# Optimization experiments

Hardware: AMD Instinct MI355X
Metric: run time of the kernel (lower is better)

The kernel has to match this reference:

```python
import jax, jax.numpy as jnp
import numpy as np

N_NODES = 100000


def gcn_conv(x, src, dst, W, b, n_nodes):
    """PyG GCNConv: add self-loops, symmetric deg^{-1/2} norm, gather-scatter."""
    h = x @ W  # [N, out]
    # add self-loops (fixed shapes)
    loop = jnp.arange(n_nodes, dtype=src.dtype)
    s = jnp.concatenate([src, loop])
    d = jnp.concatenate([dst, loop])
    # degree on destination (includes self-loop)
    deg = jax.ops.segment_sum(jnp.ones_like(d, dtype=h.dtype), d, num_segments=n_nodes)
    dinv = jnp.where(deg > 0, jax.lax.rsqrt(deg), 0.0)
    norm = dinv[s] * dinv[d]  # [E+N]
    msg = h[s] * norm[:, None]  # gather + scale, [E+N, out]
    out = jax.ops.segment_sum(msg, d, num_segments=n_nodes)  # scatter-add
    return out + b


def setup_inputs() -> dict:
    key = jax.random.key(0)
    ks = jax.random.split(key, 10)
    n, in_d, hid, out_d, e = N_NODES, 64, 128, 64, 1600000
    x = jax.random.normal(ks[0], (n, in_d), dtype=jnp.float32)
    edge_index = jax.random.randint(ks[1], (2, e), 0, n, dtype=jnp.int64)
    s = 0.05
    return {
        "x": x,
        "edge_index": edge_index,
        "W1": jax.random.normal(ks[2], (in_d, hid), dtype=jnp.float32) * s,
        "b1": jnp.zeros((hid,), dtype=jnp.float32),
        "W2": jax.random.normal(ks[3], (hid, out_d), dtype=jnp.float32) * s,
        "b2": jnp.zeros((out_d,), dtype=jnp.float32),
        "Wd": jax.random.normal(ks[4], (out_d, 1), dtype=jnp.float32) * s,
        "bd": jnp.zeros((1,), dtype=jnp.float32),
        "Wp": jax.random.normal(ks[5], (out_d, 1), dtype=jnp.float32) * s,
        "bp": jnp.zeros((1,), dtype=jnp.float32),
    }


def reference(x, edge_index, W1, b1, W2, b2, Wd, bd, Wp, bp):
    src, dst = edge_index[0], edge_index[1]
    n = x.shape[0]
    h = jax.nn.relu(gcn_conv(x, src, dst, W1, b1, n))
    h = jax.nn.relu(gcn_conv(h, src, dst, W2, b2, n))
    duration_out = h @ Wd + bd  # [N, 1]
    phase_out = h @ Wp + bp     # [N, 1]
    return (duration_out, phase_out)
```

## Files before the change

kernel.cpp:

```cpp
#include <hip/hip_runtime.h>
#include <cstdint>
#include <cstddef>


#define MAXC 512
#define CAP  6144
#define SEG  3456
#define GPAD 16

typedef __attribute__((ext_vector_type(8))) short bf16x8;
typedef __attribute__((ext_vector_type(4))) float f32x4;

__device__ __forceinline__ float blo(unsigned int u) {
  return __uint_as_float(u << 16);
}
__device__ __forceinline__ float bhi(unsigned int u) {
  return __uint_as_float(u & 0xffff0000u);
}
__device__ __forceinline__ unsigned short f2b(float f) {
  unsigned int u = __float_as_uint(f);
  unsigned int r = u + 0x7fffu + ((u >> 16) & 1u);
  return (unsigned short)(r >> 16);
}

__global__ __launch_bounds__(256) void k_cast(const float* __restrict__ x,
                                              const float* __restrict__ dinv,
                                              unsigned int* __restrict__ xh,
                                              int n16) {
  int i = blockIdx.x * 256 + threadIdx.x;
  if (i >= n16) return;
  float di = dinv[i >> 4];
  float4 v = reinterpret_cast<const float4*>(x)[i];
  uint2 o;
  o.x = (unsigned int)f2b(v.x * di) | ((unsigned int)f2b(v.y * di) << 16);
  o.y = (unsigned int)f2b(v.z * di) | ((unsigned int)f2b(v.w * di) << 16);
  reinterpret_cast<uint2*>(xh)[i] = o;
}

__global__ void k_binit(int* __restrict__ gcur, int nc) {
  int b = blockIdx.x * 256 + threadIdx.x;
  if (b < nc) gcur[b * GPAD] = b * CAP;
}

__global__ __launch_bounds__(256) void k_pass1(const int* __restrict__ src,
                                               const int* __restrict__ dst,
                                               int* __restrict__ gcur,
                                               int* __restrict__ P,
                                               int E, int nc, int seg) {
  __shared__ int hist[MAXC];
  __shared__ int lofs[MAXC];
  __shared__ int base[MAXC];
  __shared__ int sbuf[SEG];
  __shared__ unsigned short dbuf[SEG];
  __shared__ int ssc[256];
  int tid = threadIdx.x;
  int start = blockIdx.x * seg;
  int end = min(E, start + seg);
  int cnt = end - start;
  if (cnt <= 0) return;
  for (int i = tid; i < MAXC; i += 256) hist[i] = 0;
  __syncthreads();
  for (int i = start + tid; i < end; i += 256)
    atomicAdd(&hist[dst[i] >> 8], 1);
  __syncthreads();
  int p0 = hist[2 * tid], p1 = hist[2 * tid + 1];
  int ps = p0 + p1;
  ssc[tid] = ps;
  __syncthreads();
  for (int off = 1; off < 256; off <<= 1) {
    int t = (tid >= off) ? ssc[tid - off] : 0;
    __syncthreads();
    ssc[tid] += t;
    __syncthreads();
  }
  int pe = ssc[tid] - ps;
  lofs[2 * tid] = pe;
  lofs[2 * tid + 1] = pe + p0;
  __syncthreads();
  for (int b = tid; b < nc; b += 256) {
    int h = hist[b];
    base[b] = (h ? atomicAdd(&gcur[b * GPAD], h) : 0) - lofs[b];
  }
  __syncthreads();
  for (int i = tid; i < MAXC; i += 256) hist[i] = lofs[i];
  __syncthreads();
  for (int i = start + tid; i < end; i += 256) {
    int d = dst[i];
    int b = d >> 8;
    int r = atomicAdd(&hist[b], 1);
    sbuf[r] = src[i] | ((d & 255) << 17);
    dbuf[r] = (unsigned short)b;
  }
  __syncthreads();
  for (int j = tid; j < cnt; j += 256) {
    P[base[dbuf[j]] + j] = sbuf[j];
  }
}

__global__ __launch_bounds__(256) void k_pass2(const int* __restrict__ P,
                                               const int* __restrict__ gcur,
                                               int* __restrict__ rs,
                                               int* __restrict__ c,
                                               float* __restrict__ dinv,
                                               int* __restrict__ col, int N) {
  __shared__ int sh[256];
  __shared__ int lcur[256];
  int tid = threadIdx.x;
  int node0 = blockIdx.x << 8;
  int begin = blockIdx.x * CAP;
  int end = gcur[blockIdx.x * GPAD];
  sh[tid] = 0;
  __syncthreads();
  for (int i = begin + tid; i < end; i += 256)
    atomicAdd(&sh[P[i] >> 17], 1);
  __syncthreads();
  int s = sh[tid];
  for (int off = 1; off < 256; off <<= 1) {
    int t = (tid >= off) ? sh[tid - off] : 0;
    __syncthreads();
    sh[tid] += t;
    __syncthreads();
  }
  int excl = sh[tid] - s;
  int node = node0 + tid;
  if (node < N) {
    rs[node] = begin + excl;
    c[node] = s;
    dinv[node] = rsqrtf((float)(s + 1));
  }
  lcur[tid] = begin + excl;
  __syncthreads();
  for (int i = begin + tid; i < end; i += 256) {
    int p = P[i];
    int pos = atomicAdd(&lcur[p >> 17], 1);
    col[pos] = p & 0x1FFFF;
  }
}

__global__ __launch_bounds__(256) void k_pull1(const unsigned int* __restrict__ xh,
                                               const float* __restrict__ x,
                                               const int* __restrict__ rs,
                                               const int* __restrict__ cnt,
                                               const int* __restrict__ col,
                                               const float* __restrict__ dinv,
                                               unsigned int* __restrict__ aggh,
                                               int n) {
  int node = (blockIdx.x * 256 + threadIdx.x) >> 6;
  int lane = threadIdx.x & 63;
  if (node >= n) return;
  int q = lane & 15;
  int grp = lane >> 4;
  int start = rs[node], m = cnt[node];
  const uint2* xr = reinterpret_cast<const uint2*>(xh);
  float4 acc = {0.f, 0.f, 0.f, 0.f};
  for (int base0 = 0; base0 < m; base0 += 64) {
    int lim = min(64, m - base0);
    int idx = (lane < lim) ? col[start + base0 + lane] : 0;
    int nt = lim >> 2;
    int t = 0;
    for (; t + 4 <= nt; t += 4) {
      int e0 = t * 4 + grp, e1 = e0 + 4, e2 = e0 + 8, e3 = e0 + 12;
      int s0 = __shfl(idx, e0), s1 = __shfl(idx, e1);
      int s2 = __shfl(idx, e2), s3 = __shfl(idx, e3);
      uint2 v0 = xr[(size_t)s0 * 16 + q];
      uint2 v1 = xr[(size_t)s1 * 16 + q];
      uint2 v2 = xr[(size_t)s2 * 16 + q];
      uint2 v3 = xr[(size_t)s3 * 16 + q];
      acc.x += (blo(v0.x) + blo(v1.x)) + (blo(v2.x) + blo(v3.x));
      acc.y += (bhi(v0.x) + bhi(v1.x)) + (bhi(v2.x) + bhi(v3.x));
      acc.z += (blo(v0.y) + blo(v1.y)) + (blo(v2.y) + blo(v3.y));
      acc.w += (bhi(v0.y) + bhi(v1.y)) + (bhi(v2.y) + bhi(v3.y));
    }
    for (; t + 2 <= nt; t += 2) {
      int e0 = t * 4 + grp, e1 = e0 + 4;
      int s0 = __shfl(idx, e0), s1 = __shfl(idx, e1);
      uint2 v0 = xr[(size_t)s0 * 16 + q];
      uint2 v1 = xr[(size_t)s1 * 16 + q];
      acc.x += blo(v0.x) + blo(v1.x); acc.y += bhi(v0.x) + bhi(v1.x);
      acc.z += blo(v0.y) + blo(v1.y); acc.w += bhi(v0.y) + bhi(v1.y);
    }
    if (t < nt) {
      int e0 = t * 4 + grp;
      int s0 = __shfl(idx, e0);
      uint2 v0 = xr[(size_t)s0 * 16 + q];
      acc.x += blo(v0.x); acc.y += bhi(v0.x);
      acc.z += blo(v0.y); acc.w += bhi(v0.y);
    }
    for (int j = nt * 4; j < lim; ++j) {
      int s0 = __shfl(idx, j);
      if (grp == (j & 3)) {
        uint2 v0 = xr[(size_t)s0 * 16 + q];
        acc.x += blo(v0.x); acc.y += bhi(v0.x);
        acc.z += blo(v0.y); acc.w += bhi(v0.y);
      }
    }
  }
  acc.x += __shfl_xor(acc.x, 16); acc.y += __shfl_xor(acc.y, 16);
  acc.z += __shfl_xor(acc.z, 16); acc.w += __shfl_xor(acc.w, 16);
  acc.x += __shfl_xor(acc.x, 32); acc.y += __shfl_xor(acc.y, 32);
  acc.z += __shfl_xor(acc.z, 32); acc.w += __shfl_xor(acc.w, 32);
  float di = dinv[node];
  float4 xs = *reinterpret_cast<const float4*>(x + (size_t)node * 64 + q * 4);
  acc.x = fmaf(di, xs.x, acc.x); acc.y = fmaf(di, xs.y, acc.y);
  acc.z = fmaf(di, xs.z, acc.z); acc.w = fmaf(di, xs.w, acc.w);
  if (lane < 16) {
    uint2 o;
    o.x = (unsigned int)f2b(acc.x * di) | ((unsigned int)f2b(acc.y * di) << 16);
    o.y = (unsigned int)f2b(acc.z * di) | ((unsigned int)f2b(acc.w * di) << 16);
    reinterpret_cast<uint2*>(aggh)[(size_t)node * 16 + q] = o;
  }
}

#define OFF_W1T 16384
#define OFF_W2T 32768
#define OFF_H1  49152
__global__ __launch_bounds__(256) void k_gemm12(
    const unsigned int* __restrict__ aggh,
    const float* __restrict__ W1, const float* __restrict__ b1,
    const float* __restrict__ W2, const float* __restrict__ dinv,
    unsigned int* __restrict__ g2h, int n) {
  __shared__ __align__(16) char smem[81920];
  int tid = threadIdx.x;
  int lane = tid & 63;
  int wid = tid >> 6;
  int lr = lane & 15, lg = lane >> 4;
  int wr = wid >> 1, wc = wid & 1;
  {
    int nrow = tid >> 1, h = tid & 1;
    unsigned int pk[16];
#pragma unroll
    for (int q = 0; q < 16; ++q) {
      unsigned short a = f2b(W1[(size_t)(h * 32 + 2 * q) * 128 + nrow]);
      unsigned short bq = f2b(W1[(size_t)(h * 32 + 2 * q + 1) * 128 + nrow]);
      pk[q] = (unsigned int)a | ((unsigned int)bq << 16);
    }
#pragma unroll
    for (int cc = 0; cc < 4; ++cc) {
      uint4 v = make_uint4(pk[cc * 4], pk[cc * 4 + 1], pk[cc * 4 + 2], pk[cc * 4 + 3]);
      int byte = nrow * 128 + ((h * 64 + cc * 16) ^ ((nrow & 7) << 4));
      *reinterpret_cast<uint4*>(smem + OFF_W1T + byte) = v;
    }
  }
  {
    int nrow = tid >> 2, qt = tid & 3;
    unsigned int pk[16];
#pragma unroll
    for (int q = 0; q < 16; ++q) {
      unsigned short a = f2b(W2[(size_t)(qt * 32 + 2 * q) * 64 + nrow]);
      unsigned short bq = f2b(W2[(size_t)(qt * 32 + 2 * q + 1) * 64 + nrow]);
      pk[q] = (unsigned int)a | ((unsigned int)bq << 16);
    }
#pragma unroll
    for (int cc = 0; cc < 4; ++cc) {
      uint4 v = make_uint4(pk[cc * 4], pk[cc * 4 + 1], pk[cc * 4 + 2], pk[cc * 4 + 3]);
      int byte = nrow * 256 + ((qt * 64 + cc * 16) ^ ((nrow & 7) << 4));
      *reinterpret_cast<uint4*>(smem + OFF_W2T + byte) = v;
    }
  }
  float bias[4];
#pragma unroll
  for (int ni = 0; ni < 4; ++ni) bias[ni] = b1[wc * 64 + ni * 16 + lr];

  int ntiles = (n + 127) >> 7;
  for (int tile = blockIdx.x; tile < ntiles; tile += gridDim.x) {
    int row0 = tile << 7;
    __syncthreads();
#pragma unroll
    for (int j = 0; j < 4; ++j) {
      int idx = tid + 256 * j;
      int r = idx >> 3, u = idx & 7;
      uint4 v = make_uint4(0u, 0u, 0u, 0u);
      int row = row0 + r;
      if (row < n) v = reinterpret_cast<const uint4*>(aggh)[(size_t)row * 8 + u];
      int byte = r * 128 + ((u * 16) ^ ((r & 7) << 4));
      *reinterpret_cast<uint4*>(smem + byte) = v;
    }
    __syncthreads();
    f32x4 acc1[4][4];
#pragma unroll
    for (int mi = 0; mi < 4; ++mi)
#pragma unroll
      for (int ni = 0; ni < 4; ++ni) {
        f32x4 z = {0.f, 0.f, 0.f, 0.f};
        acc1[mi][ni] = z;
      }
#pragma unroll
    for (int kk = 0; kk < 2; ++kk) {
      int kb = kk * 64 + lg * 16;
      bf16x8 af[4], bfq[4];
#pragma unroll
      for (int mi = 0; mi < 4; ++mi) {
        int r = wr * 64 + mi * 16 + lr;
        af[mi] = *reinterpret_cast<const bf16x8*>(smem + r * 128 + (kb ^ ((r & 7) << 4)));
      }
#pragma unroll
      for (int ni = 0; ni < 4; ++ni) {
        int nr = wc * 64 + ni * 16 + lr;
        bfq[ni] = *reinterpret_cast<const bf16x8*>(smem + OFF_W1T + nr * 128 + (kb ^ ((nr & 7) << 4)));
      }
#pragma unroll
      for (int mi = 0; mi < 4; ++mi)
#pragma unroll
        for (int ni = 0; ni < 4; ++ni)
          acc1[mi][ni] = __builtin_amdgcn_mfma_f32_16x16x32_bf16(
              af[mi], bfq[ni], acc1[mi][ni], 0, 0, 0);
    }
#pragma unroll
    for (int mi = 0; mi < 4; ++mi) {
      int m0 = wr * 64 + mi * 16 + lg * 4;
#pragma unroll
      for (int ni = 0; ni < 4; ++ni) {
        int kcol = wc * 64 + ni * 16 + lr;
#pragma unroll
        for (int rj = 0; rj < 4; ++rj) {
          float v = fmaxf(acc1[mi][ni][rj] + bias[ni], 0.f);
          int mm = m0 + rj;
          int byte = mm * 256 + ((kcol * 2) ^ ((mm & 15) << 4));
          *reinterpret_cast<unsigned short*>(smem + OFF_H1 + byte) = f2b(v);
        }
      }
    }
    __syncthreads();
    f32x4 acc2[4][2];
#pragma unroll
    for (int mi = 0; mi < 4; ++mi)
#pragma unroll
      for (int ni = 0; ni < 2; ++ni) {
        f32x4 z = {0.f, 0.f, 0.f, 0.f};
        acc2[mi][ni] = z;
      }
#pragma unroll
    for (int kk = 0; kk < 4; ++kk) {
      int kb = kk * 64 + lg * 16;
      bf16x8 af[4], bfq[2];
#pragma unroll
      for (int mi = 0; mi < 4; ++mi) {
        int m = wr * 64 + mi * 16 + lr;
        af[mi] = *reinterpret_cast<const bf16x8*>(smem + OFF_H1 + m * 256 + (kb ^ ((m & 15) << 4)));
      }
#pragma unroll
      for (int ni = 0; ni < 2; ++ni) {
        int nr = wc * 32 + ni * 16 + lr;
        bfq[ni] = *reinterpret_cast<const bf16x8*>(smem + OFF_W2T + nr * 256 + (kb ^ ((nr & 7) << 4)));
      }
#pragma unroll
      for (int mi = 0; mi < 4; ++mi)
#pragma unroll
        for (int ni = 0; ni < 2; ++ni)
          acc2[mi][ni] = __builtin_amdgcn_mfma_f32_16x16x32_bf16(
              af[mi], bfq[ni], acc2[mi][ni], 0, 0, 0);
    }
    __syncthreads();
#pragma unroll
    for (int mi = 0; mi < 4; ++mi) {
      int m0 = wr * 64 + mi * 16 + lg * 4;
#pragma unroll
      for (int ni = 0; ni < 2; ++ni) {
        int nn = wc * 32 + ni * 16 + lr;
#pragma unroll
        for (int rj = 0; rj < 4; ++rj) {
          int mm = m0 + rj;
          int byte = mm * 256 + ((nn * 4) ^ ((mm & 15) << 4));
          *reinterpret_cast<float*>(smem + OFF_H1 + byte) = acc2[mi][ni][rj];
        }
      }
    }
    __syncthreads();
#pragma unroll
    for (int j = 0; j < 8; ++j) {
      int idx = tid + 256 * j;
      int r = idx >> 4, c4 = idx & 15;
      int row = row0 + r;
      if (row < n) {
        float4 v = *reinterpret_cast<const float4*>(
            smem + OFF_H1 + r * 256 + ((c4 * 16) ^ ((r & 15) << 4)));
        float di = dinv[row];
        uint2 o;
        o.x = (unsigned int)f2b(v.x * di) | ((unsigned int)f2b(v.y * di) << 16);
        o.y = (unsigned int)f2b(v.z * di) | ((unsigned int)f2b(v.w * di) << 16);
        reinterpret_cast<uint2*>(g2h)[(size_t)row * 16 + c4] = o;
      }
    }
  }
}

__global__ __launch_bounds__(256) void k_pull2(const unsigned int* __restrict__ g2h,
                                               const int* __restrict__ rs,
                                               const int* __restrict__ cnt,
                                               const int* __restrict__ col,
                                               const float* __restrict__ dinv,
                                               const float* __restrict__ b,
                                               const float* __restrict__ Wd,
                                               const float* __restrict__ Wp,
                                               const float* __restrict__ bd,
                                               const float* __restrict__ bp,
                                               float* __restrict__ out, int n) {
  int node = (blockIdx.x * 256 + threadIdx.x) >> 6;
  int lane = threadIdx.x & 63;
  if (node >= n) return;
  int q = lane & 15;
  int grp = lane >> 4;
  int start = rs[node], m = cnt[node];
  const uint2* gr = reinterpret_cast<const uint2*>(g2h);
  float4 acc = {0.f, 0.f, 0.f, 0.f};
  for (int base0 = 0; base0 < m; base0 += 64) {
    int lim = min(64, m - base0);
    int idx = (lane < lim) ? col[start + base0 + lane] : 0;
    int nt = lim >> 2;
    int t = 0;
    for (; t + 4 <= nt; t += 4) {
      int e0 = t * 4 + grp, e1 = e0 + 4, e2 = e0 + 8, e3 = e0 + 12;
      int s0 = __shfl(idx, e0), s1 = __shfl(idx, e1);
      int s2 = __shfl(idx, e2), s3 = __shfl(idx, e3);
      uint2 v0 = gr[(size_t)s0 * 16 + q];
      uint2 v1 = gr[(size_t)s1 * 16 + q];
      uint2 v2 = gr[(size_t)s2 * 16 + q];
      uint2 v3 = gr[(size_t)s3 * 16 + q];
      acc.x += (blo(v0.x) + blo(v1.x)) + (blo(v2.x) + blo(v3.x));
      acc.y += (bhi(v0.x) + bhi(v1.x)) + (bhi(v2.x) + bhi(v3.x));
      acc.z += (blo(v0.y) + blo(v1.y)) + (blo(v2.y) + blo(v3.y));
      acc.w += (bhi(v0.y) + bhi(v1.y)) + (bhi(v2.y) + bhi(v3.y));
    }
    for (; t + 2 <= nt; t += 2) {
      int e0 = t * 4 + grp, e1 = e0 + 4;
      int s0 = __shfl(idx, e0), s1 = __shfl(idx, e1);
      uint2 v0 = gr[(size_t)s0 * 16 + q];
      uint2 v1 = gr[(size_t)s1 * 16 + q];
      acc.x += blo(v0.x) + blo(v1.x); acc.y += bhi(v0.x) + bhi(v1.x);
      acc.z += blo(v0.y) + blo(v1.y); acc.w += bhi(v0.y) + bhi(v1.y);
    }
    if (t < nt) {
      int e0 = t * 4 + grp;
      int s0 = __shfl(idx, e0);
      uint2 v0 = gr[(size_t)s0 * 16 + q];
      acc.x += blo(v0.x); acc.y += bhi(v0.x);
      acc.z += blo(v0.y); acc.w += bhi(v0.y);
    }
    for (int j = nt * 4; j < lim; ++j) {
      int s0 = __shfl(idx, j);
      if (grp == (j & 3)) {
        uint2 v0 = gr[(size_t)s0 * 16 + q];
        acc.x += blo(v0.x); acc.y += bhi(v0.x);
        acc.z += blo(v0.y); acc.w += bhi(v0.y);
      }
    }
  }
  acc.x += __shfl_xor(acc.x, 16); acc.y += __shfl_xor(acc.y, 16);
  acc.z += __shfl_xor(acc.z, 16); acc.w += __shfl_xor(acc.w, 16);
  acc.x += __shfl_xor(acc.x, 32); acc.y += __shfl_xor(acc.y, 32);
  acc.z += __shfl_xor(acc.z, 32); acc.w += __shfl_xor(acc.w, 32);
  {
    uint2 sv = gr[(size_t)node * 16 + q];
    acc.x += blo(sv.x); acc.y += bhi(sv.x);
    acc.z += blo(sv.y); acc.w += bhi(sv.y);
  }
  float di = dinv[node];
  float4 b4 = *reinterpret_cast<const float4*>(b + q * 4);
  float4 wd4 = *reinterpret_cast<const float4*>(Wd + q * 4);
  float4 wp4 = *reinterpret_cast<const float4*>(Wp + q * 4);
  float vx = fmaxf(fmaf(acc.x, di, b4.x), 0.f);
  float vy = fmaxf(fmaf(acc.y, di, b4.y), 0.f);
  float vz = fmaxf(fmaf(acc.z, di, b4.z), 0.f);
  float vw = fmaxf(fmaf(acc.w, di, b4.w), 0.f);
  float dsum = vx * wd4.x + vy * wd4.y + vz * wd4.z + vw * wd4.w;
  float psum = vx * wp4.x + vy * wp4.y + vz * wp4.z + vw * wp4.w;
#pragma unroll
  for (int off = 1; off < 16; off <<= 1) {
    dsum += __shfl_xor(dsum, off);
    psum += __shfl_xor(psum, off);
  }
  if (lane == 0) {
    out[node] = dsum + bd[0];
    out[n + node] = psum + bp[0];
  }
}

extern "C" void kernel_launch(void* const* d_in, const int* in_sizes, int n_in,
                              void* d_out, int out_size, void* d_ws, size_t ws_size,
                              hipStream_t stream) {
  const float* x  = (const float*)d_in[0];
  const int*   ei = (const int*)d_in[1];
  const float* W1 = (const float*)d_in[2];
  const float* b1 = (const float*)d_in[3];
  const float* W2 = (const float*)d_in[4];
  const float* b2 = (const float*)d_in[5];
  const float* Wd = (const float*)d_in[6];
  const float* bd = (const float*)d_in[7];
  const float* Wp = (const float*)d_in[8];
  const float* bp = (const float*)d_in[9];
  float* out = (float*)d_out;

  const int N = in_sizes[0] / 64;
  const int E = in_sizes[1] / 2;
  const int* src = ei;
  const int* dst = ei + E;
  const int nc = (N + 255) >> 8;

  char* ws = (char*)d_ws;
  size_t off = 0;
  auto alloc = [&](size_t bytes) -> void* {
    size_t a = (off + 255) & ~(size_t)255;
    off = a + bytes;
    return (void*)(ws + a);
  };

  int*   gcur = (int*)alloc((size_t)MAXC * GPAD * 4);
  int*   rs   = (int*)alloc((size_t)N * 4);
  int*   c    = (int*)alloc((size_t)N * 4);
  float* dinv = (float*)alloc((size_t)N * 4);
  int*   P    = (int*)alloc((size_t)nc * CAP * 4);
  int*   col  = (int*)alloc((size_t)nc * CAP * 4);
  unsigned int* xh   = (unsigned int*)alloc((size_t)N * 64 * 2);
  unsigned int* aggh = (unsigned int*)alloc((size_t)N * 64 * 2);
  unsigned int* g2h  = (unsigned int*)alloc((size_t)N * 64 * 2);
  (void)ws_size; (void)n_in; (void)out_size;

  k_binit<<<(nc + 255) / 256, 256, 0, stream>>>(gcur, nc);

  int nb1 = 512;
  int seg = (E + nb1 - 1) / nb1;
  while (seg > SEG) { nb1 *= 2; seg = (E + nb1 - 1) / nb1; }
  k_pass1<<<nb1, 256, 0, stream>>>(src, dst, gcur, P, E, nc, seg);
  k_pass2<<<nc, 256, 0, stream>>>(P, gcur, rs, c, dinv, col, N);

  k_cast<<<(N * 16 + 255) / 256, 256, 0, stream>>>(x, dinv, xh, N * 16);
  k_pull1<<<(N + 3) / 4, 256, 0, stream>>>(xh, x, rs, c, col, dinv, aggh, N);
  k_gemm12<<<512, 256, 0, stream>>>(aggh, W1, b1, W2, dinv, g2h, N);
  k_pull2<<<(N + 3) / 4, 256, 0, stream>>>(g2h, rs, c, col, dinv, b2, Wd, Wp, bd, bp, out, N);
}
```

Baseline: 258.8 us.

## Map one 16-lane group per node in pull kernels, drop wave reductions

Both gather kernels now assign a 16-lane group to each node instead of a full 64-lane wave, so each group walks the node's edge list directly with 8-way unrolled loads. This removes the per-chunk index shuffles, tail handling and cross-group xor reductions, and raises the number of nodes per block. In pull1 the self-loop term is read from the bf16 pre-scaled features instead of the fp32 input, dropping one load stream at a small precision cost. Index math also drops 64-bit casts.

```diff
diff --git a/kernel.cpp b/kernel.cpp
--- a/kernel.cpp
+++ b/kernel.cpp
@@ -138,76 +138,63 @@
 }
 
 __global__ __launch_bounds__(256) void k_pull1(const unsigned int* __restrict__ xh,
-                                               const float* __restrict__ x,
                                                const int* __restrict__ rs,
                                                const int* __restrict__ cnt,
                                                const int* __restrict__ col,
                                                const float* __restrict__ dinv,
                                                unsigned int* __restrict__ aggh,
                                                int n) {
-  int node = (blockIdx.x * 256 + threadIdx.x) >> 6;
-  int lane = threadIdx.x & 63;
-  if (node >= n) return;
-  int q = lane & 15;
-  int grp = lane >> 4;
-  int start = rs[node], m = cnt[node];
+  int tid = threadIdx.x;
+  int q = tid & 15;
+  int node = (blockIdx.x * 256 + tid) >> 4;
+  bool valid = node < n;
+  int nidx = valid ? node : 0;
+  int start = rs[nidx];
+  int m = valid ? cnt[nidx] : 0;
   const uint2* xr = reinterpret_cast<const uint2*>(xh);
+  const int* cp = col + start;
   float4 acc = {0.f, 0.f, 0.f, 0.f};
-  for (int base0 = 0; base0 < m; base0 += 64) {
-    int lim = min(64, m - base0);
-    int idx = (lane < lim) ? col[start + base0 + lane] : 0;
-    int nt = lim >> 2;
-    int t = 0;
-    for (; t + 4 <= nt; t += 4) {
-      int e0 = t * 4 + grp, e1 = e0 + 4, e2 = e0 + 8, e3 = e0 + 12;
-      int s0 = __shfl(idx, e0), s1 = __shfl(idx, e1);
-      int s2 = __shfl(idx, e2), s3 = __shfl(idx, e3);
-      uint2 v0 = xr[(size_t)s0 * 16 + q];
-      uint2 v1 = xr[(size_t)s1 * 16 + q];
-      uint2 v2 = xr[(size_t)s2 * 16 + q];
-      uint2 v3 = xr[(size_t)s3 * 16 + q];
-      acc.x += (blo(v0.x) + blo(v1.x)) + (blo(v2.x) + blo(v3.x));
-      acc.y += (bhi(v0.x) + bhi(v1.x)) + (bhi(v2.x) + bhi(v3.x));
-      acc.z += (blo(v0.y) + blo(v1.y)) + (blo(v2.y) + blo(v3.y));
-      acc.w += (bhi(v0.y) + bhi(v1.y)) + (bhi(v2.y) + bhi(v3.y));
-    }
-    for (; t + 2 <= nt; t += 2) {
-      int e0 = t * 4 + grp, e1 = e0 + 4;
-      int s0 = __shfl(idx, e0), s1 = __shfl(idx, e1);
-      uint2 v0 = xr[(size_t)s0 * 16 + q];
-      uint2 v1 = xr[(size_t)s1 * 16 + q];
-      acc.x += blo(v0.x) + blo(v1.x); acc.y += bhi(v0.x) + bhi(v1.x);
-      acc.z += blo(v0.y) + blo(v1.y); acc.w += bhi(v0.y) + bhi(v1.y);
-    }
-    if (t < nt) {
-      int e0 = t * 4 + grp;
-      int s0 = __shfl(idx, e0);
-      uint2 v0 = xr[(size_t)s0 * 16 + q];
-      acc.x += blo(v0.x); acc.y += bhi(v0.x);
-      acc.z += blo(v0.y); acc.w += bhi(v0.y);
-    }
-    for (int j = nt * 4; j < lim; ++j) {
-      int s0 = __shfl(idx, j);
-      if (grp == (j & 3)) {
-        uint2 v0 = xr[(size_t)s0 * 16 + q];
-        acc.x += blo(v0.x); acc.y += bhi(v0.x);
-        acc.z += blo(v0.y); acc.w += bhi(v0.y);
-      }
-    }
-  }
-  acc.x += __shfl_xor(acc.x, 16); acc.y += __shfl_xor(acc.y, 16);
-  acc.z += __shfl_xor(acc.z, 16); acc.w += __shfl_xor(acc.w, 16);
-  acc.x += __shfl_xor(acc.x, 32); acc.y += __shfl_xor(acc.y, 32);
-  acc.z += __shfl_xor(acc.z, 32); acc.w += __shfl_xor(acc.w, 32);
-  float di = dinv[node];
-  float4 xs = *reinterpret_cast<const float4*>(x + (size_t)node * 64 + q * 4);
-  acc.x = fmaf(di, xs.x, acc.x); acc.y = fmaf(di, xs.y, acc.y);
-  acc.z = fmaf(di, xs.z, acc.z); acc.w = fmaf(di, xs.w, acc.w);
-  if (lane < 16) {
+  int t = 0;
+  for (; t + 8 <= m; t += 8) {
+    int i0 = cp[t],     i1 = cp[t + 1], i2 = cp[t + 2], i3 = cp[t + 3];
+    int i4 = cp[t + 4], i5 = cp[t + 5], i6 = cp[t + 6], i7 = cp[t + 7];
+    uint2 v0 = xr[i0 * 16 + q], v1 = xr[i1 * 16 + q];
+    uint2 v2 = xr[i2 * 16 + q], v3 = xr[i3 * 16 + q];
+    uint2 v4 = xr[i4 * 16 + q], v5 = xr[i5 * 16 + q];
+    uint2 v6 = xr[i6 * 16 + q], v7 = xr[i7 * 16 + q];
+    acc.x += ((blo(v0.x) + blo(v1.x)) + (blo(v2.x) + blo(v3.x)))
+           + ((blo(v4.x) + blo(v5.x)) + (blo(v6.x) + blo(v7.x)));
+    acc.y += ((bhi(v0.x) + bhi(v1.x)) + (bhi(v2.x) + bhi(v3.x)))
+           + ((bhi(v4.x) + bhi(v5.x)) + (bhi(v6.x) + bhi(v7.x)));
+    acc.z += ((blo(v0.y) + blo(v1.y)) + (blo(v2.y) + blo(v3.y)))
+           + ((blo(v4.y) + blo(v5.y)) + (blo(v6.y) + blo(v7.y)));
+    acc.w += ((bhi(v0.y) + bhi(v1.y)) + (bhi(v2.y) + bhi(v3.y)))
+           + ((bhi(v4.y) + bhi(v5.y)) + (bhi(v6.y) + bhi(v7.y)));
+  }
+  for (; t + 4 <= m; t += 4) {
+    int i0 = cp[t], i1 = cp[t + 1], i2 = cp[t + 2], i3 = cp[t + 3];
+    uint2 v0 = xr[i0 * 16 + q], v1 = xr[i1 * 16 + q];
+    uint2 v2 = xr[i2 * 16 + q], v3 = xr[i3 * 16 + q];
+    acc.x += (blo(v0.x) + blo(v1.x)) + (blo(v2.x) + blo(v3.x));
+    acc.y += (bhi(v0.x) + bhi(v1.x)) + (bhi(v2.x) + bhi(v3.x));
+    acc.z += (blo(v0.y) + blo(v1.y)) + (blo(v2.y) + blo(v3.y));
+    acc.w += (bhi(v0.y) + bhi(v1.y)) + (bhi(v2.y) + bhi(v3.y));
+  }
+  for (; t < m; ++t) {
+    int i0 = cp[t];
+    uint2 v0 = xr[i0 * 16 + q];
+    acc.x += blo(v0.x); acc.y += bhi(v0.x);
+    acc.z += blo(v0.y); acc.w += bhi(v0.y);
+  }
+  if (valid) {
+    uint2 sv = xr[node * 16 + q];
+    acc.x += blo(sv.x); acc.y += bhi(sv.x);
+    acc.z += blo(sv.y); acc.w += bhi(sv.y);
+    float di = dinv[node];
     uint2 o;
     o.x = (unsigned int)f2b(acc.x * di) | ((unsigned int)f2b(acc.y * di) << 16);
     o.y = (unsigned int)f2b(acc.z * di) | ((unsigned int)f2b(acc.w * di) << 16);
-    reinterpret_cast<uint2*>(aggh)[(size_t)node * 16 + q] = o;
+    reinterpret_cast<uint2*>(aggh)[node * 16 + q] = o;
   }
 }
 
@@ -395,66 +382,54 @@
                                                const float* __restrict__ bd,
                                                const float* __restrict__ bp,
                                                float* __restrict__ out, int n) {
-  int node = (blockIdx.x * 256 + threadIdx.x) >> 6;
-  int lane = threadIdx.x & 63;
-  if (node >= n) return;
-  int q = lane & 15;
-  int grp = lane >> 4;
-  int start = rs[node], m = cnt[node];
+  int tid = threadIdx.x;
+  int q = tid & 15;
+  int node = (blockIdx.x * 256 + tid) >> 4;
+  bool valid = node < n;
+  int nidx = valid ? node : 0;
+  int start = rs[nidx];
+  int m = valid ? cnt[nidx] : 0;
   const uint2* gr = reinterpret_cast<const uint2*>(g2h);
+  const int* cp = col + start;
   float4 acc = {0.f, 0.f, 0.f, 0.f};
-  for (int base0 = 0; base0 < m; base0 += 64) {
-    int lim = min(64, m - base0);
-    int idx = (lane < lim) ? col[start + base0 + lane] : 0;
-    int nt = lim >> 2;
-    int t = 0;
-    for (; t + 4 <= nt; t += 4) {
-      int e0 = t * 4 + grp, e1 = e0 + 4, e2 = e0 + 8, e3 = e0 + 12;
-      int s0 = __shfl(idx, e0), s1 = __shfl(idx, e1);
-      int s2 = __shfl(idx, e2), s3 = __shfl(idx, e3);
-      uint2 v0 = gr[(size_t)s0 * 16 + q];
-      uint2 v1 = gr[(size_t)s1 * 16 + q];
-      uint2 v2 = gr[(size_t)s2 * 16 + q];
-      uint2 v3 = gr[(size_t)s3 * 16 + q];
-      acc.x += (blo(v0.x) + blo(v1.x)) + (blo(v2.x) + blo(v3.x));
-      acc.y += (bhi(v0.x) + bhi(v1.x)) + (bhi(v2.x) + bhi(v3.x));
-      acc.z += (blo(v0.y) + blo(v1.y)) + (blo(v2.y) + blo(v3.y));
-      acc.w += (bhi(v0.y) + bhi(v1.y)) + (bhi(v2.y) + bhi(v3.y));
-    }
-    for (; t + 2 <= nt; t += 2) {
-      int e0 = t * 4 + grp, e1 = e0 + 4;
-      int s0 = __shfl(idx, e0), s1 = __shfl(idx, e1);
-      uint2 v0 = gr[(size_t)s0 * 16 + q];
-      uint2 v1 = gr[(size_t)s1 * 16 + q];
-      acc.x += blo(v0.x) + blo(v1.x); acc.y += bhi(v0.x) + bhi(v1.x);
-      acc.z += blo(v0.y) + blo(v1.y); acc.w += bhi(v0.y) + bhi(v1.y);
-    }
-    if (t < nt) {
-      int e0 = t * 4 + grp;
-      int s0 = __shfl(idx, e0);
-      uint2 v0 = gr[(size_t)s0 * 16 + q];
-      acc.x += blo(v0.x); acc.y += bhi(v0.x);
-      acc.z += blo(v0.y); acc.w += bhi(v0.y);
-    }
-    for (int j = nt * 4; j < lim; ++j) {
-      int s0 = __shfl(idx, j);
-      if (grp == (j & 3)) {
-        uint2 v0 = gr[(size_t)s0 * 16 + q];
-        acc.x += blo(v0.x); acc.y += bhi(v0.x);
-        acc.z += blo(v0.y); acc.w += bhi(v0.y);
-      }
-    }
-  }
-  acc.x += __shfl_xor(acc.x, 16); acc.y += __shfl_xor(acc.y, 16);
-  acc.z += __shfl_xor(acc.z, 16); acc.w += __shfl_xor(acc.w, 16);
-  acc.x += __shfl_xor(acc.x, 32); acc.y += __shfl_xor(acc.y, 32);
-  acc.z += __shfl_xor(acc.z, 32); acc.w += __shfl_xor(acc.w, 32);
+  int t = 0;
+  for (; t + 8 <= m; t += 8) {
+    int i0 = cp[t],     i1 = cp[t + 1], i2 = cp[t + 2], i3 = cp[t + 3];
+    int i4 = cp[t + 4], i5 = cp[t + 5], i6 = cp[t + 6], i7 = cp[t + 7];
+    uint2 v0 = gr[i0 * 16 + q], v1 = gr[i1 * 16 + q];
+    uint2 v2 = gr[i2 * 16 + q], v3 = gr[i3 * 16 + q];
+    uint2 v4 = gr[i4 * 16 + q], v5 = gr[i5 * 16 + q];
+    uint2 v6 = gr[i6 * 16 + q], v7 = gr[i7 * 16 + q];
+    acc.x += ((blo(v0.x) + blo(v1.x)) + (blo(v2.x) + blo(v3.x)))
+           + ((blo(v4.x) + blo(v5.x)) + (blo(v6.x) + blo(v7.x)));
+    acc.y += ((bhi(v0.x) + bhi(v1.x)) + (bhi(v2.x) + bhi(v3.x)))
+           + ((bhi(v4.x) + bhi(v5.x)) + (bhi(v6.x) + bhi(v7.x)));
+    acc.z += ((blo(v0.y) + blo(v1.y)) + (blo(v2.y) + blo(v3.y)))
+           + ((blo(v4.y) + blo(v5.y)) + (blo(v6.y) + blo(v7.y)));
+    acc.w += ((bhi(v0.y) + bhi(v1.y)) + (bhi(v2.y) + bhi(v3.y)))
+           + ((bhi(v4.y) + bhi(v5.y)) + (bhi(v6.y) + bhi(v7.y)));
+  }
+  for (; t + 4 <= m; t += 4) {
+    int i0 = cp[t], i1 = cp[t + 1], i2 = cp[t + 2], i3 = cp[t + 3];
+    uint2 v0 = gr[i0 * 16 + q], v1 = gr[i1 * 16 + q];
+    uint2 v2 = gr[i2 * 16 + q], v3 = gr[i3 * 16 + q];
+    acc.x += (blo(v0.x) + blo(v1.x)) + (blo(v2.x) + blo(v3.x));
+    acc.y += (bhi(v0.x) + bhi(v1.x)) + (bhi(v2.x) + bhi(v3.x));
+    acc.z += (blo(v0.y) + blo(v1.y)) + (blo(v2.y) + blo(v3.y));
+    acc.w += (bhi(v0.y) + bhi(v1.y)) + (bhi(v2.y) + bhi(v3.y));
+  }
+  for (; t < m; ++t) {
+    int i0 = cp[t];
+    uint2 v0 = gr[i0 * 16 + q];
+    acc.x += blo(v0.x); acc.y += bhi(v0.x);
+    acc.z += blo(v0.y); acc.w += bhi(v0.y);
+  }
   {
-    uint2 sv = gr[(size_t)node * 16 + q];
+    uint2 sv = gr[nidx * 16 + q];
     acc.x += blo(sv.x); acc.y += bhi(sv.x);
     acc.z += blo(sv.y); acc.w += bhi(sv.y);
   }
-  float di = dinv[node];
+  float di = dinv[nidx];
   float4 b4 = *reinterpret_cast<const float4*>(b + q * 4);
   float4 wd4 = *reinterpret_cast<const float4*>(Wd + q * 4);
   float4 wp4 = *reinterpret_cast<const float4*>(Wp + q * 4);
@@ -469,7 +444,7 @@
     dsum += __shfl_xor(dsum, off);
     psum += __shfl_xor(psum, off);
   }
-  if (lane == 0) {
+  if (valid && q == 0) {
     out[node] = dsum + bd[0];
     out[n + node] = psum + bp[0];
   }
@@ -524,7 +499,7 @@
   k_pass2<<<nc, 256, 0, stream>>>(P, gcur, rs, c, dinv, col, N);
 
   k_cast<<<(N * 16 + 255) / 256, 256, 0, stream>>>(x, dinv, xh, N * 16);
-  k_pull1<<<(N + 3) / 4, 256, 0, stream>>>(xh, x, rs, c, col, dinv, aggh, N);
+  k_pull1<<<(N + 15) / 16, 256, 0, stream>>>(xh, rs, c, col, dinv, aggh, N);
   k_gemm12<<<512, 256, 0, stream>>>(aggh, W1, b1, W2, dinv, g2h, N);
-  k_pull2<<<(N + 3) / 4, 256, 0, stream>>>(g2h, rs, c, col, dinv, b2, Wd, Wp, bd, bp, out, N);
-}
+  k_pull2<<<(N + 15) / 16, 256, 0, stream>>>(g2h, rs, c, col, dinv, b2, Wd, Wp, bd, bp, out, N);
+}
```

Result: faster. 222.2 us (-14.2%).
